# Kernel tuning notes

Measured on AMD Instinct MI355X. Metric: run time of the kernel, lower is better.

The kernel has to match this reference:

```python
import jax, jax.numpy as jnp
import numpy as np

N_HEAD = 16


def setup_inputs() -> dict:
    key = jax.random.key(0)
    k1, k2, k3 = jax.random.split(key, 3)
    B, T, C = 2, 2048, 1024
    x = jax.random.normal(k1, (B, T, C), dtype=jnp.float32)
    Wqkv = jax.random.normal(k2, (C, 3 * C), dtype=jnp.float32) * 0.02
    bqkv = jnp.zeros((3 * C,), dtype=jnp.float32)
    Wproj = jax.random.normal(k3, (C, C), dtype=jnp.float32) * 0.02
    bproj = jnp.zeros((C,), dtype=jnp.float32)
    return {"x": x, "Wqkv": Wqkv, "bqkv": bqkv, "Wproj": Wproj, "bproj": bproj}


def reference(x, Wqkv, bqkv, Wproj, bproj):
    b, t, c = x.shape
    h = N_HEAD
    d = c // h  # head_dim
    # qkv projection, split into q,k,v per head: (b,t,3,h,d)
    qkv = (x @ Wqkv + bqkv).reshape(b, t, 3, h, d)
    q, k, v = qkv[:, :, 0], qkv[:, :, 1], qkv[:, :, 2]  # each (b,t,h,d)
    # Faithful quirk of original: n_state = head_dim // heads, scale = 1/sqrt(n_state)
    scale = jnp.float32(1.0 / np.sqrt(d // h))
    # attn_mode == 'all': dense non-causal attention
    w = jnp.einsum('bqhd,bkhd->bhqk', q, k)  # (b,h,t,t)
    w = jax.nn.softmax(w * scale, axis=-1)
    a = jnp.einsum('bhqk,bkhd->bqhd', w, v).reshape(b, t, c)
    return a @ Wproj + bproj
```

## Files before the change

### kernel.cpp

```cpp
#include <hip/hip_runtime.h>

typedef float floatx4 __attribute__((ext_vector_type(4)));
typedef float floatx16 __attribute__((ext_vector_type(16)));
typedef __bf16 bf16x8 __attribute__((ext_vector_type(8)));
typedef __bf16 bf16x4 __attribute__((ext_vector_type(4)));
typedef __bf16 bf16x2 __attribute__((ext_vector_type(2)));
typedef float floatx2 __attribute__((ext_vector_type(2)));

#define MFMA16 __builtin_amdgcn_mfma_f32_16x16x32_bf16
#define MFMA32 __builtin_amdgcn_mfma_f32_32x32x16_bf16

typedef const __attribute__((address_space(1))) void* gas_t;
typedef __attribute__((address_space(3))) void* las_t;
#define GLD16(g, l) __builtin_amdgcn_global_load_lds((gas_t)(g), (las_t)(l), 16, 0, 0)

static __device__ __forceinline__ unsigned short f2bf(float f) {
  union { float f; unsigned int u; } v; v.f = f;
  unsigned int r = v.u + 0x7fffu + ((v.u >> 16) & 1u);
  return (unsigned short)(r >> 16);
}

static __device__ __forceinline__ unsigned pk2(float a, float b) {
  floatx2 v; v[0] = a; v[1] = b;
  union { bf16x2 h; unsigned u; } u;
  u.h = __builtin_convertvector(v, bf16x2);
  return u.u;
}

static __device__ __forceinline__ void cast_transpose_tile(
    const float* __restrict__ in, unsigned short* __restrict__ out,
    int R, int C, int bx, int by) {
  const int r0 = by * 64, c0 = bx * 64;
  const int tid = threadIdx.x;
  __shared__ float tl[64][65];
  const int rr = tid >> 4, cc = (tid & 15) * 4;
#pragma unroll
  for (int i = 0; i < 4; ++i) {
    int row = rr + i * 16;
    float4 v = *(const float4*)(in + (size_t)(r0 + row) * C + c0 + cc);
    tl[row][cc] = v.x; tl[row][cc + 1] = v.y;
    tl[row][cc + 2] = v.z; tl[row][cc + 3] = v.w;
  }
  __syncthreads();
  const int cl = tid >> 2, rbase = (tid & 3) * 16;
  unsigned short o[16];
#pragma unroll
  for (int j = 0; j < 16; ++j) o[j] = f2bf(tl[rbase + j][cl]);
  unsigned short* dst = out + (size_t)(c0 + cl) * R + r0 + rbase;
  *(uint4*)dst = *(uint4*)o;
  *(uint4*)(dst + 8) = *(uint4*)(o + 8);
}

__global__ __launch_bounds__(256) void prologue_kernel(
    const float* __restrict__ x, unsigned short* __restrict__ Xb,
    const float* __restrict__ Wqkv, unsigned short* __restrict__ Wqkvt,
    const float* __restrict__ Wproj, unsigned short* __restrict__ Wprojt) {
  const int bid = blockIdx.x;
  if (bid < 4096) {
    int i = bid * 256 + threadIdx.x;
    float4 v = ((const float4*)x)[i];
    ushort4 o;
    o.x = f2bf(v.x); o.y = f2bf(v.y); o.z = f2bf(v.z); o.w = f2bf(v.w);
    ((ushort4*)Xb)[i] = o;
  } else if (bid < 4096 + 768) {
    int b2 = bid - 4096;
    cast_transpose_tile(Wqkv, Wqkvt, 1024, 3072, b2 % 48, b2 / 48);
  } else {
    int b3 = bid - 4096 - 768;
    cast_transpose_tile(Wproj, Wprojt, 1024, 1024, b3 % 16, b3 / 16);
  }
}

__global__ __launch_bounds__(256) void gemm_qkv(
    const unsigned short* __restrict__ A,
    const unsigned short* __restrict__ Bt,
    const float* __restrict__ bias,
    unsigned short* __restrict__ Q,
    unsigned short* __restrict__ Kc,
    unsigned short* __restrict__ Vt) {
  const int K = 1024;
  const int m0 = blockIdx.y * 128, n0 = blockIdx.x * 128;
  const int tid = threadIdx.x, w = tid >> 6, l = tid & 63;
  const int l16 = l & 15, lq = l >> 4;
  const int wm = w >> 1, wn = w & 1;
  const int which = n0 >> 10;

  __shared__ __align__(16) unsigned short SH[16384];
  unsigned short* As = SH;
  unsigned short* Bs = SH + 8192;

  floatx4 acc[4][4] = {};

  int sA[4], sB[4];
  unsigned ldso[4];
#pragma unroll
  for (int j = 0; j < 4; ++j) {
    int s = j * 256 + tid;
    int row = s >> 3, blk = (s & 7) ^ (row & 7);
    sA[j] = (m0 + row) * K + blk * 8;
    sB[j] = (n0 + row) * K + blk * 8;
    ldso[j] = (unsigned)(j * 256 + w * 64) * 8;
  }

  if (which == 2) {
    for (int k0 = 0; k0 < K; k0 += 64) {
      __syncthreads();
#pragma unroll
      for (int j = 0; j < 4; ++j) {
        GLD16(A + sA[j] + k0, As + ldso[j]);
        GLD16(Bt + sB[j] + k0, Bs + ldso[j]);
      }
      __syncthreads();
#pragma unroll
      for (int kk = 0; kk < 2; ++kk) {
        bf16x8 af[4], bf[4];
#pragma unroll
        for (int mi = 0; mi < 4; ++mi) {
          int row = wm * 64 + mi * 16 + l16;
          int blk = (kk * 4 + lq) ^ (l16 & 7);
          af[mi] = *(const bf16x8*)(As + row * 64 + blk * 8);
        }
#pragma unroll
        for (int ni = 0; ni < 4; ++ni) {
          int row = wn * 64 + ni * 16 + l16;
          int blk = (kk * 4 + lq) ^ (l16 & 7);
          bf[ni] = *(const bf16x8*)(Bs + row * 64 + blk * 8);
        }
#pragma unroll
        for (int ni = 0; ni < 4; ++ni)
#pragma unroll
          for (int mi = 0; mi < 4; ++mi)
            acc[mi][ni] = MFMA16(af[mi], bf[ni], acc[mi][ni], 0, 0, 0);
      }
    }
    float bv[4];
#pragma unroll
    for (int ni = 0; ni < 4; ++ni) bv[ni] = bias[n0 + wn * 64 + ni * 16 + l16];
    __syncthreads();
    unsigned short* E = SH + w * 2304;
    const int bh = (m0 >> 11) * 16 + ((n0 & 1023) >> 6) + wn;
    const int tt0 = (m0 & 2047) + wm * 64;
#pragma unroll
    for (int p = 0; p < 2; ++p) {
#pragma unroll
      for (int n2 = 0; n2 < 2; ++n2) {
        int ni = p * 2 + n2;
#pragma unroll
        for (int mi = 0; mi < 4; ++mi) {
          floatx4 vv = acc[mi][ni] + bv[ni];
          *(bf16x4*)(E + (n2 * 16 + l16) * 72 + mi * 16 + lq * 4) =
              __builtin_convertvector(vv, bf16x4);
        }
      }
#pragma unroll
      for (int s = 0; s < 4; ++s) {
        int dl = s * 8 + (l >> 3);
        bf16x8 vv = *(const bf16x8*)(E + dl * 72 + (l & 7) * 8);
        *(bf16x8*)(Vt + ((size_t)bh * 64 + p * 32 + dl) * 2048 + tt0 +
                   (l & 7) * 8) = vv;
      }
    }
  } else {
    for (int k0 = 0; k0 < K; k0 += 64) {
      __syncthreads();
#pragma unroll
      for (int j = 0; j < 4; ++j) {
        GLD16(A + sA[j] + k0, As + ldso[j]);
        GLD16(Bt + sB[j] + k0, Bs + ldso[j]);
      }
      __syncthreads();
#pragma unroll
      for (int kk = 0; kk < 2; ++kk) {
        bf16x8 af[4], bf[4];
#pragma unroll
        for (int mi = 0; mi < 4; ++mi) {
          int row = wm * 64 + mi * 16 + l16;
          int blk = (kk * 4 + lq) ^ (l16 & 7);
          af[mi] = *(const bf16x8*)(As + row * 64 + blk * 8);
        }
#pragma unroll
        for (int ni = 0; ni < 4; ++ni) {
          int row = wn * 64 + ni * 16 + l16;
          int blk = (kk * 4 + lq) ^ (l16 & 7);
          bf[ni] = *(const bf16x8*)(Bs + row * 64 + blk * 8);
        }
#pragma unroll
        for (int ni = 0; ni < 4; ++ni)
#pragma unroll
          for (int mi = 0; mi < 4; ++mi)
            acc[mi][ni] = MFMA16(bf[ni], af[mi], acc[mi][ni], 0, 0, 0);
      }
    }
    const float sc = (which == 0) ? 0.7213475204444817f : 1.0f;
    unsigned short* dst = (which == 0) ? Q : Kc;
    __syncthreads();
    unsigned short* E = SH + w * 2304;
    const int bh = (m0 >> 11) * 16 + ((n0 & 1023) >> 6) + wn;
    const size_t gbase = ((size_t)bh * 2048 + (m0 & 2047) + wm * 64) * 64;
#pragma unroll
    for (int p = 0; p < 2; ++p) {
#pragma unroll
      for (int m2 = 0; m2 < 2; ++m2) {
        int mi = p * 2 + m2;
#pragma unroll
        for (int ni = 0; ni < 4; ++ni) {
          int col0 = n0 + wn * 64 + ni * 16 + lq * 4;
          floatx4 bv = *(const floatx4*)(bias + col0);
          floatx4 vv = (acc[mi][ni] + bv) * sc;
          *(bf16x4*)(E + (m2 * 16 + l16) * 72 + ni * 16 + lq * 4) =
              __builtin_convertvector(vv, bf16x4);
        }
      }
#pragma unroll
      for (int s = 0; s < 4; ++s) {
        int rl = s * 8 + (l >> 3);
        bf16x8 vv = *(const bf16x8*)(E + rl * 72 + (l & 7) * 8);
        *(bf16x8*)(dst + gbase + (size_t)(p * 32 + rl) * 64 + (l & 7) * 8) =
            vv;
      }
    }
  }
}

__global__ __launch_bounds__(256, 2) void attn_kernel(
    const unsigned short* __restrict__ Q,
    const unsigned short* __restrict__ Kc,
    const unsigned short* __restrict__ Vt,
    unsigned short* __restrict__ AO) {
  const int T = 2048;
  const int bh = blockIdx.y, q0 = blockIdx.x * 128;
  const int tid = threadIdx.x, w = tid >> 6, l = tid & 63;
  const int r31 = l & 31, g = l >> 5;

  __shared__ __align__(16) unsigned short KVs[2][2][4096];

  bf16x8 qf[4];
  {
    const unsigned short* qr =
        Q + ((size_t)bh * T + q0 + w * 32 + r31) * 64 + g * 8;
#pragma unroll
    for (int ds = 0; ds < 4; ++ds) qf[ds] = *(const bf16x8*)(qr + ds * 16);
  }

  floatx16 o_acc[2] = {};
  float l_lane = 0.f;

  const unsigned short* kbase = Kc + (size_t)bh * T * 64;
  const unsigned short* vbase = Vt + (size_t)bh * 64 * T;
  int kro[2], vro[2];
  unsigned ldso[2];
#pragma unroll
  for (int j = 0; j < 2; ++j) {
    int s = j * 256 + tid;
    int row = s >> 3, blk = (s & 7) ^ (row & 7);
    kro[j] = row * 64 + blk * 8;
    vro[j] = row * T + blk * 8;
    ldso[j] = (unsigned)(j * 256 + (tid & 192)) * 8;
  }

#pragma unroll
  for (int j = 0; j < 2; ++j) {
    GLD16(kbase + kro[j], &KVs[0][0][ldso[j]]);
    GLD16(vbase + vro[j], &KVs[0][1][ldso[j]]);
  }

  for (int c = 0; c < 32; ++c) {
    __syncthreads();
    if (c < 31) {
      const int nb = (c + 1) & 1;
#pragma unroll
      for (int j = 0; j < 2; ++j) {
        GLD16(kbase + (c + 1) * 4096 + kro[j], &KVs[nb][0][ldso[j]]);
        GLD16(vbase + (c + 1) * 64 + vro[j], &KVs[nb][1][ldso[j]]);
      }
    }
    const unsigned short* kb = KVs[c & 1][0];
    const unsigned short* vb = KVs[c & 1][1];

    floatx16 sac[2];
#pragma unroll
    for (int kt = 0; kt < 2; ++kt) {
      const int row = kt * 32 + r31, rx = row & 7;
      const unsigned short* kr = kb + row * 64;
      floatx16 z = {};
#pragma unroll
      for (int ds = 0; ds < 4; ++ds)
        z = MFMA32(*(const bf16x8*)(kr + ((ds * 2 + g) ^ rx) * 8), qf[ds], z,
                   0, 0, 0);
      sac[kt] = z;
    }

    bf16x8 pf[4];
#pragma unroll
    for (int kt = 0; kt < 2; ++kt) {
      float p[16];
#pragma unroll
      for (int r = 0; r < 16; ++r) p[r] = __builtin_amdgcn_exp2f(sac[kt][r]);
      l_lane += (((p[0] + p[1]) + (p[2] + p[3])) +
                 ((p[4] + p[5]) + (p[6] + p[7]))) +
                (((p[8] + p[9]) + (p[10] + p[11])) +
                 ((p[12] + p[13]) + (p[14] + p[15])));
#pragma unroll
      for (int s2 = 0; s2 < 2; ++s2) {
        unsigned cA = pk2(p[8 * s2 + 0], p[8 * s2 + 1]);
        unsigned cB = pk2(p[8 * s2 + 2], p[8 * s2 + 3]);
        unsigned cC = pk2(p[8 * s2 + 4], p[8 * s2 + 5]);
        unsigned cD = pk2(p[8 * s2 + 6], p[8 * s2 + 7]);
        unsigned xA = (unsigned)__shfl_xor((int)cA, 32, 64);
        unsigned xB = (unsigned)__shfl_xor((int)cB, 32, 64);
        unsigned xC = (unsigned)__shfl_xor((int)cC, 32, 64);
        unsigned xD = (unsigned)__shfl_xor((int)cD, 32, 64);
        union { unsigned u[4]; bf16x8 v; } pu;
        pu.u[0] = g ? xC : cA;
        pu.u[1] = g ? xD : cB;
        pu.u[2] = g ? cC : xA;
        pu.u[3] = g ? cD : xB;
        pf[kt * 2 + s2] = pu.v;
      }
    }

#pragma unroll
    for (int dt = 0; dt < 2; ++dt) {
      const int row = dt * 32 + r31, rx = row & 7;
      const unsigned short* vr = vb + row * 64;
#pragma unroll
      for (int s = 0; s < 4; ++s) {
        bf16x8 vf = *(const bf16x8*)(vr + ((s * 2 + g) ^ rx) * 8);
        o_acc[dt] = MFMA32(vf, pf[s], o_acc[dt], 0, 0, 0);
      }
    }
  }

  float ls = l_lane + __shfl_xor(l_lane, 32, 64);
  float inv = 1.0f / ls;
  const int b = bh >> 4, h = bh & 15;
  const int t = q0 + w * 32 + r31;
  unsigned short* ao = AO + ((size_t)b * 2048 + t) * 1024 + h * 64;
#pragma unroll
  for (int dt = 0; dt < 2; ++dt)
#pragma unroll
    for (int rq = 0; rq < 4; ++rq) {
      floatx4 ov;
      ov[0] = o_acc[dt][rq * 4 + 0]; ov[1] = o_acc[dt][rq * 4 + 1];
      ov[2] = o_acc[dt][rq * 4 + 2]; ov[3] = o_acc[dt][rq * 4 + 3];
      ov *= inv;
      *(bf16x4*)(ao + dt * 32 + rq * 8 + g * 4) =
          __builtin_convertvector(ov, bf16x4);
    }
}

__global__ __launch_bounds__(256) void gemm_proj(
    const unsigned short* __restrict__ A,
    const unsigned short* __restrict__ Bt,
    const float* __restrict__ bias,
    float* __restrict__ out) {
  const int K = 1024, N = 1024;
  const int m0 = blockIdx.y * 128, n0 = blockIdx.x * 64;
  const int tid = threadIdx.x, w = tid >> 6, l = tid & 63;
  const int l16 = l & 15, lq = l >> 4;

  __shared__ __align__(16) unsigned short As[128 * 64];
  __shared__ __align__(16) unsigned short Bs[64 * 64];

  floatx4 acc[2][4] = {};

  int sA[4], sB[2];
  unsigned ldsoA[4], ldsoB[2];
#pragma unroll
  for (int j = 0; j < 4; ++j) {
    int s = j * 256 + tid;
    int row = s >> 3, blk = (s & 7) ^ (row & 7);
    sA[j] = (m0 + row) * K + blk * 8;
    ldsoA[j] = (unsigned)(j * 256 + w * 64) * 8;
  }
#pragma unroll
  for (int j = 0; j < 2; ++j) {
    int s = j * 256 + tid;
    int row = s >> 3, blk = (s & 7) ^ (row & 7);
    sB[j] = (n0 + row) * K + blk * 8;
    ldsoB[j] = (unsigned)(j * 256 + w * 64) * 8;
  }

  for (int k0 = 0; k0 < K; k0 += 64) {
    __syncthreads();
#pragma unroll
    for (int j = 0; j < 4; ++j) GLD16(A + sA[j] + k0, As + ldsoA[j]);
#pragma unroll
    for (int j = 0; j < 2; ++j) GLD16(Bt + sB[j] + k0, Bs + ldsoB[j]);
    __syncthreads();
#pragma unroll
    for (int kk = 0; kk < 2; ++kk) {
      bf16x8 af[2], bf[4];
#pragma unroll
      for (int mi = 0; mi < 2; ++mi) {
        int row = w * 32 + mi * 16 + l16;
        int blk = (kk * 4 + lq) ^ (l16 & 7);
        af[mi] = *(const bf16x8*)(As + row * 64 + blk * 8);
      }
#pragma unroll
      for (int ni = 0; ni < 4; ++ni) {
        int row = ni * 16 + l16;
        int blk = (kk * 4 + lq) ^ (l16 & 7);
        bf[ni] = *(const bf16x8*)(Bs + row * 64 + blk * 8);
      }
#pragma unroll
      for (int ni = 0; ni < 4; ++ni)
#pragma unroll
        for (int mi = 0; mi < 2; ++mi)
          acc[mi][ni] = MFMA16(bf[ni], af[mi], acc[mi][ni], 0, 0, 0);
    }
  }

#pragma unroll
  for (int mi = 0; mi < 2; ++mi) {
    int t = m0 + w * 32 + mi * 16 + l16;
#pragma unroll
    for (int ni = 0; ni < 4; ++ni) {
      int col0 = n0 + ni * 16 + lq * 4;
      floatx4 bv = *(const floatx4*)(bias + col0);
      *(floatx4*)(out + (size_t)t * N + col0) = acc[mi][ni] + bv;
    }
  }
}

extern "C" void kernel_launch(void* const* d_in, const int* in_sizes, int n_in,
                              void* d_out, int out_size, void* d_ws,
                              size_t ws_size, hipStream_t stream) {
  const float* x     = (const float*)d_in[0];
  const float* Wqkv  = (const float*)d_in[1];
  const float* bqkv  = (const float*)d_in[2];
  const float* Wproj = (const float*)d_in[3];
  const float* bproj = (const float*)d_in[4];
  float* out = (float*)d_out;

  unsigned short* Xb     = (unsigned short*)d_ws;
  unsigned short* Wqkvt  = Xb + 4194304;
  unsigned short* Wprojt = Wqkvt + 3145728;
  unsigned short* Qb     = Wprojt + 1048576;
  unsigned short* Kb     = Qb + 4194304;
  unsigned short* Vtb    = Kb + 4194304;
  unsigned short* AOb    = Vtb + 4194304;

  prologue_kernel<<<5120, 256, 0, stream>>>(x, Xb, Wqkv, Wqkvt, Wproj, Wprojt);
  gemm_qkv<<<dim3(24, 32), 256, 0, stream>>>(Xb, Wqkvt, bqkv, Qb, Kb, Vtb);
  attn_kernel<<<dim3(16, 32), 256, 0, stream>>>(Qb, Kb, Vtb, AOb);
  gemm_proj<<<dim3(16, 32), 256, 0, stream>>>(AOb, Wprojt, bproj, out);
}
```

Baseline: 190.7 us.

## Permute V layout in QKV epilogue to drop P shuffles; double KV tile per barrier

The QKV GEMM epilogue now writes V^T with its key (time) columns permuted inside each 64-wide chunk. This lets the attention kernel pack exp(S) results straight into bf16 MFMA operands without the cross-half __shfl_xor exchanges. The attention loop also stages two 64-key chunks per buffer (16 periods instead of 32), which halves the number of barriers and doubles shared memory to 64KB per block. The larger LDS footprint may reduce occupancy at two blocks per CU.

New measurement: 184.5 us. -3.3%, faster.

```diff
diff --git a/kernel.cpp b/kernel.cpp
--- a/kernel.cpp
+++ b/kernel.cpp
@@ -140,6 +140,7 @@
     unsigned short* E = SH + w * 2304;
     const int bh = (m0 >> 11) * 16 + ((n0 & 1023) >> 6) + wn;
     const int tt0 = (m0 & 2047) + wm * 64;
+    const int m8 = l & 7, bc = 16 * (m8 >> 1) + 4 * (m8 & 1);
 #pragma unroll
     for (int p = 0; p < 2; ++p) {
 #pragma unroll
@@ -155,9 +156,11 @@
 #pragma unroll
       for (int s = 0; s < 4; ++s) {
         int dl = s * 8 + (l >> 3);
-        bf16x8 vv = *(const bf16x8*)(E + dl * 72 + (l & 7) * 8);
+        union { bf16x4 h[2]; bf16x8 v; } uu;
+        uu.h[0] = *(const bf16x4*)(E + dl * 72 + bc);
+        uu.h[1] = *(const bf16x4*)(E + dl * 72 + bc + 8);
         *(bf16x8*)(Vt + ((size_t)bh * 64 + p * 32 + dl) * 2048 + tt0 +
-                   (l & 7) * 8) = vv;
+                   m8 * 8) = uu.v;
       }
     }
   } else {
@@ -232,7 +235,7 @@
   const int tid = threadIdx.x, w = tid >> 6, l = tid & 63;
   const int r31 = l & 31, g = l >> 5;
 
-  __shared__ __align__(16) unsigned short KVs[2][2][4096];
+  __shared__ __align__(16) unsigned short KVs[2][2][2][4096];
 
   bf16x8 qf[4];
   {
@@ -258,78 +261,73 @@
     ldso[j] = (unsigned)(j * 256 + (tid & 192)) * 8;
   }
 
-#pragma unroll
-  for (int j = 0; j < 2; ++j) {
-    GLD16(kbase + kro[j], &KVs[0][0][ldso[j]]);
-    GLD16(vbase + vro[j], &KVs[0][1][ldso[j]]);
-  }
-
-  for (int c = 0; c < 32; ++c) {
+#define STAGE_PERIOD(pp, nb)                                              \
+  {                                                                       \
+    _Pragma("unroll") for (int c2 = 0; c2 < 2; ++c2) {                    \
+      const int c = (pp) * 2 + c2;                                        \
+      _Pragma("unroll") for (int j = 0; j < 2; ++j) {                     \
+        GLD16(kbase + c * 4096 + kro[j], &KVs[nb][0][c2][ldso[j]]);       \
+        GLD16(vbase + c * 64 + vro[j], &KVs[nb][1][c2][ldso[j]]);         \
+      }                                                                   \
+    }                                                                     \
+  }
+
+  STAGE_PERIOD(0, 0);
+
+  for (int p = 0; p < 16; ++p) {
     __syncthreads();
-    if (c < 31) {
-      const int nb = (c + 1) & 1;
-#pragma unroll
-      for (int j = 0; j < 2; ++j) {
-        GLD16(kbase + (c + 1) * 4096 + kro[j], &KVs[nb][0][ldso[j]]);
-        GLD16(vbase + (c + 1) * 64 + vro[j], &KVs[nb][1][ldso[j]]);
-      }
-    }
-    const unsigned short* kb = KVs[c & 1][0];
-    const unsigned short* vb = KVs[c & 1][1];
-
-    floatx16 sac[2];
-#pragma unroll
-    for (int kt = 0; kt < 2; ++kt) {
-      const int row = kt * 32 + r31, rx = row & 7;
-      const unsigned short* kr = kb + row * 64;
-      floatx16 z = {};
-#pragma unroll
-      for (int ds = 0; ds < 4; ++ds)
-        z = MFMA32(*(const bf16x8*)(kr + ((ds * 2 + g) ^ rx) * 8), qf[ds], z,
-                   0, 0, 0);
-      sac[kt] = z;
-    }
-
-    bf16x8 pf[4];
-#pragma unroll
-    for (int kt = 0; kt < 2; ++kt) {
-      float p[16];
-#pragma unroll
-      for (int r = 0; r < 16; ++r) p[r] = __builtin_amdgcn_exp2f(sac[kt][r]);
-      l_lane += (((p[0] + p[1]) + (p[2] + p[3])) +
-                 ((p[4] + p[5]) + (p[6] + p[7]))) +
-                (((p[8] + p[9]) + (p[10] + p[11])) +
-                 ((p[12] + p[13]) + (p[14] + p[15])));
-#pragma unroll
-      for (int s2 = 0; s2 < 2; ++s2) {
-        unsigned cA = pk2(p[8 * s2 + 0], p[8 * s2 + 1]);
-        unsigned cB = pk2(p[8 * s2 + 2], p[8 * s2 + 3]);
-        unsigned cC = pk2(p[8 * s2 + 4], p[8 * s2 + 5]);
-        unsigned cD = pk2(p[8 * s2 + 6], p[8 * s2 + 7]);
-        unsigned xA = (unsigned)__shfl_xor((int)cA, 32, 64);
-        unsigned xB = (unsigned)__shfl_xor((int)cB, 32, 64);
-        unsigned xC = (unsigned)__shfl_xor((int)cC, 32, 64);
-        unsigned xD = (unsigned)__shfl_xor((int)cD, 32, 64);
-        union { unsigned u[4]; bf16x8 v; } pu;
-        pu.u[0] = g ? xC : cA;
-        pu.u[1] = g ? xD : cB;
-        pu.u[2] = g ? cC : xA;
-        pu.u[3] = g ? cD : xB;
-        pf[kt * 2 + s2] = pu.v;
-      }
-    }
-
-#pragma unroll
-    for (int dt = 0; dt < 2; ++dt) {
-      const int row = dt * 32 + r31, rx = row & 7;
-      const unsigned short* vr = vb + row * 64;
-#pragma unroll
-      for (int s = 0; s < 4; ++s) {
-        bf16x8 vf = *(const bf16x8*)(vr + ((s * 2 + g) ^ rx) * 8);
-        o_acc[dt] = MFMA32(vf, pf[s], o_acc[dt], 0, 0, 0);
-      }
-    }
-  }
+    if (p < 15) {
+      const int nb = (p + 1) & 1;
+      STAGE_PERIOD(p + 1, nb);
+    }
+    const int pb = p & 1;
+#pragma unroll
+    for (int c2 = 0; c2 < 2; ++c2) {
+      const unsigned short* kb = &KVs[pb][0][c2][0];
+      const unsigned short* vb = &KVs[pb][1][c2][0];
+
+      bf16x8 pf[4];
+#pragma unroll
+      for (int kt = 0; kt < 2; ++kt) {
+        const int row = kt * 32 + r31, rx = row & 7;
+        const unsigned short* kr = kb + row * 64;
+        floatx16 z = {};
+#pragma unroll
+        for (int ds = 0; ds < 4; ++ds)
+          z = MFMA32(*(const bf16x8*)(kr + ((ds * 2 + g) ^ rx) * 8), qf[ds],
+                     z, 0, 0, 0);
+
+        float pe[16];
+#pragma unroll
+        for (int r = 0; r < 16; ++r) pe[r] = __builtin_amdgcn_exp2f(z[r]);
+        l_lane += (((pe[0] + pe[1]) + (pe[2] + pe[3])) +
+                   ((pe[4] + pe[5]) + (pe[6] + pe[7]))) +
+                  (((pe[8] + pe[9]) + (pe[10] + pe[11])) +
+                   ((pe[12] + pe[13]) + (pe[14] + pe[15])));
+#pragma unroll
+        for (int s2 = 0; s2 < 2; ++s2) {
+          union { unsigned u[4]; bf16x8 v; } pu;
+          pu.u[0] = pk2(pe[8 * s2 + 0], pe[8 * s2 + 1]);
+          pu.u[1] = pk2(pe[8 * s2 + 2], pe[8 * s2 + 3]);
+          pu.u[2] = pk2(pe[8 * s2 + 4], pe[8 * s2 + 5]);
+          pu.u[3] = pk2(pe[8 * s2 + 6], pe[8 * s2 + 7]);
+          pf[kt * 2 + s2] = pu.v;
+        }
+      }
+
+#pragma unroll
+      for (int dt = 0; dt < 2; ++dt) {
+        const int row = dt * 32 + r31, rx = row & 7;
+        const unsigned short* vr = vb + row * 64;
+#pragma unroll
+        for (int s = 0; s < 4; ++s) {
+          bf16x8 vf = *(const bf16x8*)(vr + ((s * 2 + g) ^ rx) * 8);
+          o_acc[dt] = MFMA32(vf, pf[s], o_acc[dt], 0, 0, 0);
+        }
+      }
+    }
+  }
+#undef STAGE_PERIOD
 
   float ls = l_lane + __shfl_xor(l_lane, 32, 64);
   float inv = 1.0f / ls;
```
